# Kernel tuning notes

Measured on AMD Instinct MI355X. Metric: run time of the kernel, lower is better.

## Reference

```python
import jax, jax.numpy as jnp
import numpy as np

N = 50000   # nodes
E = 800000  # edges (avg degree 16)
D = 128     # in_dim = out_dim
H = 8       # heads
O = D // H  # per-head dim = 16
FF = 512    # ffn inner hidden
LN_EPS = 1e-6
LRELU_SLOPE = 0.01  # torch F.leaky_relu default


def setup_inputs() -> dict:
    key = jax.random.key(0)
    ks = jax.random.split(key, 9)
    x = jax.random.normal(ks[0], (N, D), jnp.float32)
    src = jax.random.randint(ks[1], (E,), 0, N)
    dst = jax.random.randint(ks[2], (E,), 0, N)
    fc_w = jax.random.normal(ks[3], (H, D, O), jnp.float32) * 0.05
    a_l = jax.random.normal(ks[4], (H, O), jnp.float32) * 0.05
    a_r = jax.random.normal(ks[5], (H, O), jnp.float32) * 0.05
    w1 = jax.random.normal(ks[6], (D, FF), jnp.float32) * 0.05
    b1 = jnp.zeros((FF,), jnp.float32)
    w2 = jax.random.normal(ks[7], (FF, D), jnp.float32) * 0.05
    b2 = jnp.zeros((D,), jnp.float32)
    ln_g = jnp.ones((D,), jnp.float32)
    ln_b = jnp.zeros((D,), jnp.float32)
    return dict(x=x, fc_w=fc_w, a_l=a_l, a_r=a_r, ln_g=ln_g, ln_b=ln_b,
                w1=w1, b1=b1, w2=w2, b2=b2, src=src, dst=dst)


def _gat_s2s(x, fc_w, a_l, a_r, src, dst):
    # per-head projection: [N,H,O]
    z = jnp.einsum('nd,hdo->nho', x, fc_w)
    # attn_fc([z_src||z_dst]) == a_l . z_src + a_r . z_dst  (decomposed, same math)
    el = jnp.einsum('nho,ho->nh', z, a_l)  # [N,H]
    er = jnp.einsum('nho,ho->nh', z, a_r)  # [N,H]
    e = jax.nn.leaky_relu(el[src] + er[dst], LRELU_SLOPE)  # [E,H]
    # edge softmax over incoming edges of each dst node (numerically stable)
    m = jax.ops.segment_max(e, dst, num_segments=N)  # [N,H]
    m = jnp.where(jnp.isfinite(m), m, 0.0)
    ex = jnp.exp(e - m[dst])  # [E,H]
    denom = jax.ops.segment_sum(ex, dst, num_segments=N)  # [N,H]
    alpha = ex / denom[dst]  # [E,H]
    # weighted aggregation of source features: [N,H,O]
    agg = jax.ops.segment_sum(alpha[:, :, None] * z[src], dst, num_segments=N)
    return agg.reshape(N, H * O)  # head concat -> [N,D]


def _ffn(h, ln_g, ln_b, w1, b1, w2, b2):
    # pre-LayerNorm positionwise FFN with gelu and residual (dropout off / eval)
    mu = jnp.mean(h, axis=-1, keepdims=True)
    var = jnp.mean((h - mu) ** 2, axis=-1, keepdims=True)
    ln = (h - mu) * jax.lax.rsqrt(var + LN_EPS) * ln_g + ln_b
    inter = jax.nn.gelu(ln @ w1 + b1, approximate=False)
    return inter @ w2 + b2 + h


def reference(x, fc_w, a_l, a_r, ln_g, ln_b, w1, b1, w2, b2, src, dst):
    h = jax.nn.elu(_gat_s2s(x, fc_w, a_l, a_r, src, dst))
    h = h + x  # residual with origin (S2S: origin == neighbor == x)
    return _ffn(h, ln_g, ln_b, w1, b1, w2, b2)
```

## Files before the change

### kernel.cpp

```cpp
#include <hip/hip_runtime.h>

#define NN 50000
#define EE 800000
#define LDK 136
#define SLOTS 64
#define FEPT 8
#define NFB 391

#define C_ZW   0
#define C_AL   16384
#define C_AR   16512
#define C_LNG  16640
#define C_LNB  16768
#define C_W1T  16896
#define C_B1   82432
#define C_W2T  82944
#define C_B2   148480
#define C_WAT  148608
#define C_TOT  150656

typedef __attribute__((ext_vector_type(8))) short bf16x8;
typedef __attribute__((ext_vector_type(4))) float f32x4;

__device__ __forceinline__ float bf2f(unsigned short u) {
  union { unsigned int i; float f; } v; v.i = ((unsigned int)u) << 16; return v.f;
}
__device__ __forceinline__ unsigned short f2bf(float f) {
  union { float f; unsigned int i; } v; v.f = f;
  unsigned int r = v.i + 0x7fffu + ((v.i >> 16) & 1u);
  return (unsigned short)(r >> 16);
}
__device__ __forceinline__ int ld_idx(const void* p, int i, int is64) {
  return is64 ? (int)((const long long*)p)[i] : ((const int*)p)[i];
}

__device__ __forceinline__ float fast_gelu(float u) {
  float ax = fabsf(u) * 0.70710678118654752f;
  float d  = fmaf(0.3275911f, ax, 1.f);
  float r  = __builtin_amdgcn_rcpf(d);
  r = r * fmaf(-d, r, 2.f);
  float p = fmaf(1.061405429f, r, -1.453152027f);
  p = fmaf(p, r, 1.421413741f);
  p = fmaf(p, r, -0.284496736f);
  p = fmaf(p, r, 0.254829592f);
  p = p * r;
  float e = __expf(-ax * ax);
  float erfv = fmaf(-p, e, 1.f);
  union { float f; unsigned int i; } su, se;
  su.f = u; se.f = erfv;
  se.i = se.i | (su.i & 0x80000000u);
  return 0.5f * u * (1.f + se.f);
}

__global__ void k_probe(const unsigned short* __restrict__ xr,
                        const int* __restrict__ s, const int* __restrict__ d,
                        int* __restrict__ flags) {
  int i = blockIdx.x * 256 + threadIdx.x;
  int bad = 0, zc = 0, zs = 0, zd = 0;
  for (int j = i; j < 65536; j += 32 * 256) {
    unsigned short u = xr[j];
    if ((u & 0x7F80u) == 0x7F80u) bad = 1;
    if (((j & 1) == 0) && u == 0) zc++;
  }
  for (int j = i; j < 131072; j += 32 * 256) {
    if (j & 1) {
      if (s[j] == 0) zs++;
      if (d[j] == 0) zd++;
    }
  }
  if (bad) atomicOr(&flags[0], 1);
  if (zc) atomicAdd(&flags[1], zc);
  if (zs) atomicAdd(&flags[2], zs);
  if (zd) atomicAdd(&flags[3], zd);
}

__global__ __launch_bounds__(256) void k_convert(
    const void* __restrict__ fcw,
    const void* __restrict__ a_l, const void* __restrict__ a_r,
    const void* __restrict__ lng, const void* __restrict__ lnb,
    const void* __restrict__ w1, const void* __restrict__ b1,
    const void* __restrict__ w2, const void* __restrict__ b2,
    const int* __restrict__ flag, unsigned short* __restrict__ canon) {
  const int isf32 = (flag[0] != 0) || (flag[1] > 8192);
  for (int i = blockIdx.x * 256 + threadIdx.x; i < C_TOT; i += gridDim.x * 256) {
    unsigned short v;
    if (i >= C_WAT) {
      int j = i - C_WAT; int c = j >> 7, dd = j & 127; int h = c & 7;
      const void* fa = (c < 8) ? a_l : a_r;
      float s = 0.f;
      if (isf32) {
        const float* fw = (const float*)fcw + h * 2048 + dd * 16;
        const float* fv = (const float*)fa + h * 16;
#pragma unroll
        for (int o = 0; o < 16; o++) s += fw[o] * fv[o];
      } else {
        const unsigned short* fw = (const unsigned short*)fcw + h * 2048 + dd * 16;
        const unsigned short* fv = (const unsigned short*)fa + h * 16;
#pragma unroll
        for (int o = 0; o < 16; o++) s += bf2f(fw[o]) * bf2f(fv[o]);
      }
      v = f2bf(s);
    } else {
      const void* src; int idx;
      if (i < C_AL)       { int c = i >> 7, d = i & 127; src = fcw; idx = (c >> 4) * 2048 + d * 16 + (c & 15); }
      else if (i < C_AR)  { src = a_l; idx = i - C_AL; }
      else if (i < C_LNG) { src = a_r; idx = i - C_AR; }
      else if (i < C_LNB) { src = lng; idx = i - C_LNG; }
      else if (i < C_W1T) { src = lnb; idx = i - C_LNB; }
      else if (i < C_B1)  { int j = i - C_W1T; int n = j >> 7, k = j & 127; src = w1; idx = k * 512 + n; }
      else if (i < C_W2T) { src = b1;  idx = i - C_B1; }
      else if (i < C_B2)  { int j = i - C_W2T; int n = j >> 9, k = j & 511; src = w2; idx = k * 128 + n; }
      else                { src = b2;  idx = i - C_B2; }
      if (isf32) v = f2bf(((const float*)src)[idx]);
      else       v = ((const unsigned short*)src)[idx];
    }
    canon[i] = v;
  }
}

__device__ __forceinline__ void do_fill(const void* __restrict__ src,
                                        const void* __restrict__ dst,
                                        const int* __restrict__ iflags,
                                        int* __restrict__ cnt,
                                        unsigned short* __restrict__ esrc,
                                        int base) {
  if (base >= EE) return;
  const int s64 = iflags[0] > 1000, d64 = iflags[1] > 1000;
  int dv[FEPT], sv[FEPT];
  if (!d64 && base + FEPT <= EE) {
    const int4* p = (const int4*)((const int*)dst + base);
    int4 a = p[0], b = p[1];
    dv[0]=a.x; dv[1]=a.y; dv[2]=a.z; dv[3]=a.w; dv[4]=b.x; dv[5]=b.y; dv[6]=b.z; dv[7]=b.w;
  } else {
#pragma unroll
    for (int j = 0; j < FEPT; j++) dv[j] = (base + j < EE) ? ld_idx(dst, base + j, d64) : 0;
  }
  if (!s64 && base + FEPT <= EE) {
    const int4* p = (const int4*)((const int*)src + base);
    int4 a = p[0], b = p[1];
    sv[0]=a.x; sv[1]=a.y; sv[2]=a.z; sv[3]=a.w; sv[4]=b.x; sv[5]=b.y; sv[6]=b.z; sv[7]=b.w;
  } else {
#pragma unroll
    for (int j = 0; j < FEPT; j++) sv[j] = (base + j < EE) ? ld_idx(src, base + j, s64) : 0;
  }
#pragma unroll
  for (int j = 0; j < FEPT; j++) {
    if (base + j < EE) {
      unsigned d = (unsigned)dv[j]; if (d >= NN) d = 0;
      unsigned s = (unsigned)sv[j]; if (s >= NN) s = 0;
      int p = atomicAdd(&cnt[d], 1);
      if (p < SLOTS) esrc[d * SLOTS + p] = (unsigned short)s;
    }
  }
}

__global__ __launch_bounds__(256) void k_projfill(
    const unsigned short* __restrict__ canon, const void* __restrict__ xraw,
    unsigned short* __restrict__ z, float* __restrict__ el, float* __restrict__ er,
    const void* __restrict__ srcp, const void* __restrict__ dstp,
    const int* __restrict__ flags,
    int* __restrict__ cnt, unsigned short* __restrict__ esrc) {
  __shared__ unsigned short sA[128 * LDK];
  __shared__ unsigned short sB[64 * LDK];
  if (blockIdx.x < NFB) {
    do_fill(srcp, dstp, flags + 2, cnt, esrc, (blockIdx.x * 256 + threadIdx.x) * FEPT);
    return;
  }
  const int pid = blockIdx.x - NFB;
  const unsigned short* zwt = canon + C_ZW;
  const unsigned short* wat = canon + C_WAT;
  const int isf32 = (flags[0] != 0) || (flags[1] > 8192);
  const int tid = threadIdx.x;
  const int row0 = (pid >> 1) * 128;
  const int n0 = (pid & 1) * 64;
  for (int v = tid; v < 2048; v += 256) {
    int r = v >> 4, k8 = (v & 15) << 3;
    int gr = row0 + r; if (gr >= NN) gr = NN - 1;
    if (isf32) {
      const float* xf = (const float*)xraw + gr * 128 + k8;
      float4 a = *(const float4*)xf;
      float4 b = *(const float4*)(xf + 4);
      union { unsigned short u[8]; uint4 q; } pk;
      pk.u[0] = f2bf(a.x); pk.u[1] = f2bf(a.y); pk.u[2] = f2bf(a.z); pk.u[3] = f2bf(a.w);
      pk.u[4] = f2bf(b.x); pk.u[5] = f2bf(b.y); pk.u[6] = f2bf(b.z); pk.u[7] = f2bf(b.w);
      *(uint4*)(&sA[r * LDK + k8]) = pk.q;
    } else {
      *(uint4*)(&sA[r * LDK + k8]) = *(const uint4*)((const unsigned short*)xraw + gr * 128 + k8);
    }
  }
  for (int v = tid; v < 1024; v += 256) {
    int n = v >> 4, k8 = (v & 15) << 3;
    *(uint4*)(&sB[n * LDK + k8]) = *(const uint4*)(zwt + (n0 + n) * 128 + k8);
  }
  __syncthreads();
  const int lane = tid & 63, w = tid >> 6;
  const int mr = lane & 15, q = lane >> 4;
  const f32x4 zero = {0.f, 0.f, 0.f, 0.f};
  f32x4 acc[8];
#pragma unroll
  for (int i = 0; i < 8; i++) acc[i] = zero;
#pragma unroll
  for (int kc = 0; kc < 4; kc++) {
    bf16x8 b = *(const bf16x8*)(&sB[(w * 16 + mr) * LDK + kc * 32 + q * 8]);
#pragma unroll
    for (int mt = 0; mt < 8; mt++) {
      bf16x8 a = *(const bf16x8*)(&sA[(mt * 16 + mr) * LDK + kc * 32 + q * 8]);
      acc[mt] = __builtin_amdgcn_mfma_f32_16x16x32_bf16(a, b, acc[mt], 0, 0, 0);
    }
  }
  const int col = n0 + w * 16 + mr;
#pragma unroll
  for (int mt = 0; mt < 8; mt++) {
#pragma unroll
    for (int r = 0; r < 4; r++) {
      int grow = row0 + mt * 16 + q * 4 + r;
      if (grow < NN) z[grow * 128 + col] = f2bf(acc[mt][r]);
    }
  }
  if (n0 == 0) {
    f32x4 e0 = zero, e1 = zero;
#pragma unroll
    for (int kc = 0; kc < 4; kc++) {
      bf16x8 b = *(const bf16x8*)(wat + mr * 128 + kc * 32 + q * 8);
      bf16x8 a0 = *(const bf16x8*)(&sA[(w * 16 + mr) * LDK + kc * 32 + q * 8]);
      bf16x8 a1 = *(const bf16x8*)(&sA[((w + 4) * 16 + mr) * LDK + kc * 32 + q * 8]);
      e0 = __builtin_amdgcn_mfma_f32_16x16x32_bf16(a0, b, e0, 0, 0, 0);
      e1 = __builtin_amdgcn_mfma_f32_16x16x32_bf16(a1, b, e1, 0, 0, 0);
    }
    float* eo = (mr < 8) ? el : er;
    const int hh = mr & 7;
#pragma unroll
    for (int r = 0; r < 4; r++) {
      int g0 = row0 + w * 16 + q * 4 + r;
      int g1 = row0 + (w + 4) * 16 + q * 4 + r;
      if (g0 < NN) eo[g0 * 8 + hh] = e0[r];
      if (g1 < NN) eo[g1 * 8 + hh] = e1[r];
    }
  }
}

__global__ __launch_bounds__(256) void k_agg(
    const void* __restrict__ xraw, const unsigned short* __restrict__ z,
    const float* __restrict__ el, const float* __restrict__ er,
    const int* __restrict__ cnt, const unsigned short* __restrict__ esrc,
    const void* __restrict__ srcp, const void* __restrict__ dstp,
    const int* __restrict__ flags,
    float* __restrict__ h1out, float2* __restrict__ mars) {
  const int lane = threadIdx.x & 63;
  const int node = blockIdx.x * 4 + (threadIdx.x >> 6);
  if (node >= NN) return;
  const int degr = cnt[node];
  const int hl = lane & 7;
  const int g  = lane >> 3;
  const float ern = er[node * 8 + hl];

  float m = -3.0e38f;
  float acc[16];
#pragma unroll
  for (int j = 0; j < 16; j++) acc[j] = 0.f;
  float denom = 0.f;

  if (degr <= SLOTS) {
    const int deg = degr;
    const unsigned short* eptr = esrc + node * SLOTS;
    for (int b = 0; b < deg; b += 16) {
      int e0 = b + g, e1 = b + g + 8;
      int c0 = (e0 < deg) ? e0 : deg - 1;
      int c1 = (e1 < deg) ? e1 : deg - 1;
      unsigned s0 = eptr[c0]; if (s0 >= NN) s0 = 0;
      unsigned s1 = eptr[c1]; if (s1 >= NN) s1 = 0;
      float t0 = el[s0 * 8 + hl] + ern;
      float t1 = el[s1 * 8 + hl] + ern;
      t0 = (t0 > 0.f) ? t0 : 0.01f * t0;
      t1 = (t1 > 0.f) ? t1 : 0.01f * t1;
      if (e0 < deg) m = fmaxf(m, t0);
      if (e1 < deg) m = fmaxf(m, t1);
    }
    m = fmaxf(m, __shfl_xor(m, 8));
    m = fmaxf(m, __shfl_xor(m, 16));
    m = fmaxf(m, __shfl_xor(m, 32));
    for (int b = 0; b < deg; b += 16) {
      int e0 = b + g, e1 = b + g + 8;
      int c0 = (e0 < deg) ? e0 : deg - 1;
      int c1 = (e1 < deg) ? e1 : deg - 1;
      unsigned s0 = eptr[c0]; if (s0 >= NN) s0 = 0;
      unsigned s1 = eptr[c1]; if (s1 >= NN) s1 = 0;
      float t0 = el[s0 * 8 + hl] + ern;
      float t1 = el[s1 * 8 + hl] + ern;
      bf16x8 za0 = *(const bf16x8*)(z + s0 * 128 + hl * 16);
      bf16x8 za1 = *(const bf16x8*)(z + s0 * 128 + hl * 16 + 8);
      bf16x8 zb0 = *(const bf16x8*)(z + s1 * 128 + hl * 16);
      bf16x8 zb1 = *(const bf16x8*)(z + s1 * 128 + hl * 16 + 8);
      t0 = (t0 > 0.f) ? t0 : 0.01f * t0;
      t1 = (t1 > 0.f) ? t1 : 0.01f * t1;
      float ex0 = (e0 < deg) ? __expf(fminf(t0 - m, 0.f)) : 0.f;
      float ex1 = (e1 < deg) ? __expf(fminf(t1 - m, 0.f)) : 0.f;
      denom += ex0 + ex1;
#pragma unroll
      for (int j = 0; j < 8; j++) {
        acc[j]     += ex0 * bf2f((unsigned short)za0[j]) + ex1 * bf2f((unsigned short)zb0[j]);
        acc[j + 8] += ex0 * bf2f((unsigned short)za1[j]) + ex1 * bf2f((unsigned short)zb1[j]);
      }
    }
  } else {
    const int s64 = flags[2] > 1000, d64 = flags[3] > 1000;
    for (int b = 0; b < EE; b += 8) {
      int e = b + g;
      unsigned dd = (unsigned)ld_idx(dstp, e, d64); if (dd >= NN) dd = 0;
      bool ok = (dd == (unsigned)node);
      unsigned s0 = (unsigned)ld_idx(srcp, e, s64); if (s0 >= NN) s0 = 0;
      float t0 = el[s0 * 8 + hl] + ern;
      t0 = (t0 > 0.f) ? t0 : 0.01f * t0;
      if (ok) m = fmaxf(m, t0);
    }
    m = fmaxf(m, __shfl_xor(m, 8));
    m = fmaxf(m, __shfl_xor(m, 16));
    m = fmaxf(m, __shfl_xor(m, 32));
    for (int b = 0; b < EE; b += 8) {
      int e = b + g;
      unsigned dd = (unsigned)ld_idx(dstp, e, d64); if (dd >= NN) dd = 0;
      bool ok = (dd == (unsigned)node);
      unsigned s0 = (unsigned)ld_idx(srcp, e, s64); if (s0 >= NN) s0 = 0;
      float t0 = el[s0 * 8 + hl] + ern;
      t0 = (t0 > 0.f) ? t0 : 0.01f * t0;
      float ex0 = ok ? __expf(fminf(t0 - m, 0.f)) : 0.f;
      denom += ex0;
      bf16x8 za0 = *(const bf16x8*)(z + s0 * 128 + hl * 16);
      bf16x8 za1 = *(const bf16x8*)(z + s0 * 128 + hl * 16 + 8);
#pragma unroll
      for (int j = 0; j < 8; j++) {
        acc[j]     += ex0 * bf2f((unsigned short)za0[j]);
        acc[j + 8] += ex0 * bf2f((unsigned short)za1[j]);
      }
    }
  }

  denom += __shfl_xor(denom, 8);
  denom += __shfl_xor(denom, 16);
  denom += __shfl_xor(denom, 32);
  {
    const bool hi1 = (lane & 32) != 0;
#pragma unroll
    for (int j = 0; j < 8; j++) {
      float send = hi1 ? acc[j] : acc[j + 8];
      float recv = __shfl_xor(send, 32);
      float keep = hi1 ? acc[j + 8] : acc[j];
      acc[j] = keep + recv;
    }
    const bool hi2 = (lane & 16) != 0;
#pragma unroll
    for (int j = 0; j < 4; j++) {
      float send = hi2 ? acc[j] : acc[j + 4];
      float recv = __shfl_xor(send, 16);
      float keep = hi2 ? acc[j + 4] : acc[j];
      acc[j] = keep + recv;
    }
    const bool hi3 = (lane & 8) != 0;
#pragma unroll
    for (int j = 0; j < 2; j++) {
      float send = hi3 ? acc[j] : acc[j + 2];
      float recv = __shfl_xor(send, 8);
      float keep = hi3 ? acc[j + 2] : acc[j];
      acc[j] = keep + recv;
    }
  }
  const float inv = (denom > 0.f) ? 1.f / denom : 0.f;
  const int c = hl * 16 + g * 2;
  float r0 = acc[0] * inv;
  float r1 = acc[1] * inv;
  float xv0, xv1;
  if ((flags[0] != 0) || (flags[1] > 8192)) {
    float2 t = *(const float2*)((const float*)xraw + (size_t)node * 128 + c);
    xv0 = t.x; xv1 = t.y;
  } else {
    unsigned int xx = *(const unsigned int*)((const unsigned short*)xraw + (size_t)node * 128 + c);
    xv0 = bf2f((unsigned short)(xx & 0xffffu));
    xv1 = bf2f((unsigned short)(xx >> 16));
  }
  float hv0 = ((r0 > 0.f) ? r0 : (__expf(fminf(r0, 0.f)) - 1.f)) + xv0;
  float hv1 = ((r1 > 0.f) ? r1 : (__expf(fminf(r1, 0.f)) - 1.f)) + xv1;
  float s1 = hv0 + hv1;
  float s2 = hv0 * hv0 + hv1 * hv1;
#pragma unroll
  for (int off = 1; off < 64; off <<= 1) {
    s1 += __shfl_xor(s1, off);
    s2 += __shfl_xor(s2, off);
  }
  if (lane == 0) {
    float mu = s1 * (1.f / 128.f);
    float var = s2 * (1.f / 128.f) - mu * mu;
    mars[node] = make_float2(mu, rsqrtf(fmaxf(var, 0.f) + 1e-6f));
  }
  *(float2*)(h1out + node * 128 + c) = make_float2(hv0, hv1);
}

__global__ __launch_bounds__(512) void k_ffn(
    const unsigned short* __restrict__ canon, const float2* __restrict__ mars,
    float* __restrict__ out) {
  const unsigned short* lngc = canon + C_LNG;
  const unsigned short* lnbc = canon + C_LNB;
  const unsigned short* w1t  = canon + C_W1T;
  const unsigned short* b1c  = canon + C_B1;
  const unsigned short* w2t  = canon + C_W2T;
  const unsigned short* b2c  = canon + C_B2;
  __shared__ unsigned short sLn[32 * LDK];
  __shared__ unsigned short sInt[32 * LDK];
  const int tid = threadIdx.x;
  const int row0 = blockIdx.x * 32;
  {
    const int r = tid >> 4, t16 = tid & 15;
    const int grow = row0 + r;
    const int gr = (grow < NN) ? grow : NN - 1;
    const float2 ms = mars[gr];
    const float* hrow = out + (size_t)gr * 128 + t16 * 8;
    float4 a = *(const float4*)(hrow);
    float4 b = *(const float4*)(hrow + 4);
    union { unsigned short u[8]; uint4 q; } gv, bv, pk;
    gv.q = *(const uint4*)(lngc + t16 * 8);
    bv.q = *(const uint4*)(lnbc + t16 * 8);
    float vv[8] = {a.x, a.y, a.z, a.w, b.x, b.y, b.z, b.w};
#pragma unroll
    for (int j = 0; j < 8; j++)
      pk.u[j] = f2bf((vv[j] - ms.x) * ms.y * bf2f(gv.u[j]) + bf2f(bv.u[j]));
    *(uint4*)(&sLn[r * LDK + t16 * 8]) = pk.q;
  }
  __syncthreads();
  const int lane = tid & 63, w = tid >> 6;
  const int mr = lane & 15, q = lane >> 4;
  const f32x4 zero = {0.f, 0.f, 0.f, 0.f};
  f32x4 acc2[2];
  acc2[0] = zero; acc2[1] = zero;
#pragma unroll
  for (int qr = 0; qr < 4; qr++) {
    if (qr) __syncthreads();
    const int colg = qr * 128 + w * 16;
    f32x4 a1[2];
    a1[0] = zero; a1[1] = zero;
#pragma unroll
    for (int kc = 0; kc < 4; kc++) {
      bf16x8 wf = *(const bf16x8*)(w1t + (colg + mr) * 128 + kc * 32 + q * 8);
#pragma unroll
      for (int rt = 0; rt < 2; rt++) {
        bf16x8 lf = *(const bf16x8*)(&sLn[(rt * 16 + mr) * LDK + kc * 32 + q * 8]);
        a1[rt] = __builtin_amdgcn_mfma_f32_16x16x32_bf16(wf, lf, a1[rt], 0, 0, 0);
      }
    }
    union { unsigned short u[4]; uint2 v; } b1v;
    b1v.v = *(const uint2*)(b1c + colg + q * 4);
#pragma unroll
    for (int rt = 0; rt < 2; rt++) {
      union { unsigned short u[4]; uint2 v; } pk;
#pragma unroll
      for (int r = 0; r < 4; r++)
        pk.u[r] = f2bf(fast_gelu(a1[rt][r] + bf2f(b1v.u[r])));
      *(uint2*)(&sInt[(rt * 16 + mr) * LDK + w * 16 + q * 4]) = pk.v;
    }
    __syncthreads();
#pragma unroll
    for (int ks = 0; ks < 4; ks++) {
      bf16x8 bw = *(const bf16x8*)(w2t + (w * 16 + mr) * 512 + qr * 128 + ks * 32 + q * 8);
#pragma unroll
      for (int mt = 0; mt < 2; mt++) {
        bf16x8 af = *(const bf16x8*)(&sInt[(mt * 16 + mr) * LDK + ks * 32 + q * 8]);
        acc2[mt] = __builtin_amdgcn_mfma_f32_16x16x32_bf16(af, bw, acc2[mt], 0, 0, 0);
      }
    }
  }
  {
    const int col = w * 16 + mr;
    const float bias = bf2f(b2c[col]);
#pragma unroll
    for (int mt = 0; mt < 2; mt++)
#pragma unroll
      for (int r = 0; r < 4; r++) {
        int grow = row0 + mt * 16 + q * 4 + r;
        if (grow < NN) {
          size_t o = (size_t)grow * 128 + col;
          out[o] = acc2[mt][r] + bias + out[o];
        }
      }
  }
}

extern "C" void kernel_launch(void* const* d_in, const int* in_sizes, int n_in,
                              void* d_out, int out_size, void* d_ws, size_t ws_size,
                              hipStream_t stream) {
  const void* x   = d_in[0];
  const void* fcw = d_in[1];
  const void* a_l = d_in[2];
  const void* a_r = d_in[3];
  const void* lng = d_in[4];
  const void* lnb = d_in[5];
  const void* w1  = d_in[6];
  const void* b1  = d_in[7];
  const void* w2  = d_in[8];
  const void* b2  = d_in[9];
  const void* src = d_in[10];
  const void* dst = d_in[11];
  float* out = (float*)d_out;

  char* ws = (char*)d_ws;
  size_t off = 0;
  auto alloc = [&](size_t bytes) -> char* {
    char* p = ws + off; off += (bytes + 255) & ~(size_t)255; return p;
  };
  int* flags            = (int*)alloc(64);
  int* cnt              = (int*)alloc((size_t)NN * 4);
  unsigned short* esrc  = (unsigned short*)alloc((size_t)NN * SLOTS * 2);
  unsigned short* canon = (unsigned short*)alloc((size_t)C_TOT * 2);
  unsigned short* z     = (unsigned short*)alloc((size_t)NN * 128 * 2);
  float* el             = (float*)alloc((size_t)NN * 8 * 4);
  float* er             = (float*)alloc((size_t)NN * 8 * 4);
  float2* mars          = (float2*)alloc((size_t)NN * 8);

  hipMemsetAsync(ws, 0, 256 + (size_t)NN * 4, stream);
  k_probe<<<32, 256, 0, stream>>>((const unsigned short*)x, (const int*)src, (const int*)dst, flags);
  k_convert<<<256, 256, 0, stream>>>(fcw, a_l, a_r, lng, lnb, w1, b1, w2, b2, flags, canon);
  k_projfill<<<NFB + 391 * 2, 256, 0, stream>>>(canon, x, z, el, er, src, dst, flags, cnt, esrc);
  k_agg<<<(NN + 3) / 4, 256, 0, stream>>>(x, z, el, er, cnt, esrc, src, dst, flags, out, mars);
  k_ffn<<<(NN + 31) / 32, 512, 0, stream>>>(canon, mars, out);
}
```

Measured before the change: 261.1 us.

## Fuse GAT aggregation with LayerNorm and FFN in one 64-row kernel

Merges the aggregation and FFN kernels. Each 512-thread block first aggregates 64 nodes (8 per wave, looping serially), applying ELU, the residual and LayerNorm, and writes the normalized rows straight to shared memory as bf16. It then runs the two MFMA GEMMs on a 64-row tile instead of 32. This removes the mars buffer, one kernel launch, and the re-read of h from global memory. In exchange, each wave now handles nodes one after another, which lowers parallelism and latency hiding in the gather-heavy phase, and the launch has far fewer blocks (782).

```diff
diff --git a/kernel.cpp b/kernel.cpp
--- a/kernel.cpp
+++ b/kernel.cpp
@@ -239,208 +239,192 @@
   }
 }
 
-__global__ __launch_bounds__(256) void k_agg(
-    const void* __restrict__ xraw, const unsigned short* __restrict__ z,
+__global__ __launch_bounds__(512) void k_aggffn(
+    const unsigned short* __restrict__ canon, const void* __restrict__ xraw,
+    const unsigned short* __restrict__ z,
     const float* __restrict__ el, const float* __restrict__ er,
     const int* __restrict__ cnt, const unsigned short* __restrict__ esrc,
     const void* __restrict__ srcp, const void* __restrict__ dstp,
-    const int* __restrict__ flags,
-    float* __restrict__ h1out, float2* __restrict__ mars) {
-  const int lane = threadIdx.x & 63;
-  const int node = blockIdx.x * 4 + (threadIdx.x >> 6);
-  if (node >= NN) return;
-  const int degr = cnt[node];
+    const int* __restrict__ flags, float* __restrict__ out) {
+  __shared__ unsigned short sLn[64 * LDK];
+  __shared__ unsigned short sInt[64 * LDK];
+  const int tid = threadIdx.x;
+  const int lane = tid & 63, w = tid >> 6;
+  const int row0 = blockIdx.x * 64;
   const int hl = lane & 7;
   const int g  = lane >> 3;
-  const float ern = er[node * 8 + hl];
-
-  float m = -3.0e38f;
-  float acc[16];
-#pragma unroll
-  for (int j = 0; j < 16; j++) acc[j] = 0.f;
-  float denom = 0.f;
-
-  if (degr <= SLOTS) {
-    const int deg = degr;
-    const unsigned short* eptr = esrc + node * SLOTS;
-    for (int b = 0; b < deg; b += 16) {
-      int e0 = b + g, e1 = b + g + 8;
-      int c0 = (e0 < deg) ? e0 : deg - 1;
-      int c1 = (e1 < deg) ? e1 : deg - 1;
-      unsigned s0 = eptr[c0]; if (s0 >= NN) s0 = 0;
-      unsigned s1 = eptr[c1]; if (s1 >= NN) s1 = 0;
-      float t0 = el[s0 * 8 + hl] + ern;
-      float t1 = el[s1 * 8 + hl] + ern;
-      t0 = (t0 > 0.f) ? t0 : 0.01f * t0;
-      t1 = (t1 > 0.f) ? t1 : 0.01f * t1;
-      if (e0 < deg) m = fmaxf(m, t0);
-      if (e1 < deg) m = fmaxf(m, t1);
-    }
-    m = fmaxf(m, __shfl_xor(m, 8));
-    m = fmaxf(m, __shfl_xor(m, 16));
-    m = fmaxf(m, __shfl_xor(m, 32));
-    for (int b = 0; b < deg; b += 16) {
-      int e0 = b + g, e1 = b + g + 8;
-      int c0 = (e0 < deg) ? e0 : deg - 1;
-      int c1 = (e1 < deg) ? e1 : deg - 1;
-      unsigned s0 = eptr[c0]; if (s0 >= NN) s0 = 0;
-      unsigned s1 = eptr[c1]; if (s1 >= NN) s1 = 0;
-      float t0 = el[s0 * 8 + hl] + ern;
-      float t1 = el[s1 * 8 + hl] + ern;
-      bf16x8 za0 = *(const bf16x8*)(z + s0 * 128 + hl * 16);
-      bf16x8 za1 = *(const bf16x8*)(z + s0 * 128 + hl * 16 + 8);
-      bf16x8 zb0 = *(const bf16x8*)(z + s1 * 128 + hl * 16);
-      bf16x8 zb1 = *(const bf16x8*)(z + s1 * 128 + hl * 16 + 8);
-      t0 = (t0 > 0.f) ? t0 : 0.01f * t0;
-      t1 = (t1 > 0.f) ? t1 : 0.01f * t1;
-      float ex0 = (e0 < deg) ? __expf(fminf(t0 - m, 0.f)) : 0.f;
-      float ex1 = (e1 < deg) ? __expf(fminf(t1 - m, 0.f)) : 0.f;
-      denom += ex0 + ex1;
+  const int c  = hl * 16 + g * 2;
+  const int isf32x = (flags[0] != 0) || (flags[1] > 8192);
+  unsigned int gq = *(const unsigned int*)(canon + C_LNG + c);
+  unsigned int bq = *(const unsigned int*)(canon + C_LNB + c);
+  const float g0 = bf2f((unsigned short)(gq & 0xffffu)), g1 = bf2f((unsigned short)(gq >> 16));
+  const float b0 = bf2f((unsigned short)(bq & 0xffffu)), b1 = bf2f((unsigned short)(bq >> 16));
+  for (int nn = 0; nn < 8; nn++) {
+    const int node0 = row0 + w * 8 + nn;
+    const int node = (node0 < NN) ? node0 : NN - 1;
+    const int degr = cnt[node];
+    const float ern = er[node * 8 + hl];
+    float m = -3.0e38f;
+    float acc[16];
+#pragma unroll
+    for (int j = 0; j < 16; j++) acc[j] = 0.f;
+    float denom = 0.f;
+    if (degr <= SLOTS) {
+      const int deg = degr;
+      const unsigned short* eptr = esrc + node * SLOTS;
+      for (int b = 0; b < deg; b += 16) {
+        int e0 = b + g, e1 = b + g + 8;
+        int c0 = (e0 < deg) ? e0 : deg - 1;
+        int c1 = (e1 < deg) ? e1 : deg - 1;
+        unsigned s0 = eptr[c0]; if (s0 >= NN) s0 = 0;
+        unsigned s1 = eptr[c1]; if (s1 >= NN) s1 = 0;
+        float t0 = el[s0 * 8 + hl] + ern;
+        float t1 = el[s1 * 8 + hl] + ern;
+        t0 = (t0 > 0.f) ? t0 : 0.01f * t0;
+        t1 = (t1 > 0.f) ? t1 : 0.01f * t1;
+        if (e0 < deg) m = fmaxf(m, t0);
+        if (e1 < deg) m = fmaxf(m, t1);
+      }
+      m = fmaxf(m, __shfl_xor(m, 8));
+      m = fmaxf(m, __shfl_xor(m, 16));
+      m = fmaxf(m, __shfl_xor(m, 32));
+      for (int b = 0; b < deg; b += 16) {
+        int e0 = b + g, e1 = b + g + 8;
+        int c0 = (e0 < deg) ? e0 : deg - 1;
+        int c1 = (e1 < deg) ? e1 : deg - 1;
+        unsigned s0 = eptr[c0]; if (s0 >= NN) s0 = 0;
+        unsigned s1 = eptr[c1]; if (s1 >= NN) s1 = 0;
+        float t0 = el[s0 * 8 + hl] + ern;
+        float t1 = el[s1 * 8 + hl] + ern;
+        bf16x8 za0 = *(const bf16x8*)(z + s0 * 128 + hl * 16);
+        bf16x8 za1 = *(const bf16x8*)(z + s0 * 128 + hl * 16 + 8);
+        bf16x8 zb0 = *(const bf16x8*)(z + s1 * 128 + hl * 16);
+        bf16x8 zb1 = *(const bf16x8*)(z + s1 * 128 + hl * 16 + 8);
+        t0 = (t0 > 0.f) ? t0 : 0.01f * t0;
+        t1 = (t1 > 0.f) ? t1 : 0.01f * t1;
+        float ex0 = (e0 < deg) ? __expf(fminf(t0 - m, 0.f)) : 0.f;
+        float ex1 = (e1 < deg) ? __expf(fminf(t1 - m, 0.f)) : 0.f;
+        denom += ex0 + ex1;
+#pragma unroll
+        for (int j = 0; j < 8; j++) {
+          acc[j]     += ex0 * bf2f((unsigned short)za0[j]) + ex1 * bf2f((unsigned short)zb0[j]);
+          acc[j + 8] += ex0 * bf2f((unsigned short)za1[j]) + ex1 * bf2f((unsigned short)zb1[j]);
+        }
+      }
+    } else {
+      const int s64 = flags[2] > 1000, d64 = flags[3] > 1000;
+      for (int b = 0; b < EE; b += 8) {
+        int e = b + g;
+        unsigned dd = (unsigned)ld_idx(dstp, e, d64); if (dd >= NN) dd = 0;
+        bool ok = (dd == (unsigned)node);
+        unsigned s0 = (unsigned)ld_idx(srcp, e, s64); if (s0 >= NN) s0 = 0;
+        float t0 = el[s0 * 8 + hl] + ern;
+        t0 = (t0 > 0.f) ? t0 : 0.01f * t0;
+        if (ok) m = fmaxf(m, t0);
+      }
+      m = fmaxf(m, __shfl_xor(m, 8));
+      m = fmaxf(m, __shfl_xor(m, 16));
+      m = fmaxf(m, __shfl_xor(m, 32));
+      for (int b = 0; b < EE; b += 8) {
+        int e = b + g;
+        unsigned dd = (unsigned)ld_idx(dstp, e, d64); if (dd >= NN) dd = 0;
+        bool ok = (dd == (unsigned)node);
+        unsigned s0 = (unsigned)ld_idx(srcp, e, s64); if (s0 >= NN) s0 = 0;
+        float t0 = el[s0 * 8 + hl] + ern;
+        t0 = (t0 > 0.f) ? t0 : 0.01f * t0;
+        float ex0 = ok ? __expf(fminf(t0 - m, 0.f)) : 0.f;
+        denom += ex0;
+        bf16x8 za0 = *(const bf16x8*)(z + s0 * 128 + hl * 16);
+        bf16x8 za1 = *(const bf16x8*)(z + s0 * 128 + hl * 16 + 8);
+#pragma unroll
+        for (int j = 0; j < 8; j++) {
+          acc[j]     += ex0 * bf2f((unsigned short)za0[j]);
+          acc[j + 8] += ex0 * bf2f((unsigned short)za1[j]);
+        }
+      }
+    }
+    denom += __shfl_xor(denom, 8);
+    denom += __shfl_xor(denom, 16);
+    denom += __shfl_xor(denom, 32);
+    {
+      const bool hi1 = (lane & 32) != 0;
 #pragma unroll
       for (int j = 0; j < 8; j++) {
-        acc[j]     += ex0 * bf2f((unsigned short)za0[j]) + ex1 * bf2f((unsigned short)zb0[j]);
-        acc[j + 8] += ex0 * bf2f((unsigned short)za1[j]) + ex1 * bf2f((unsigned short)zb1[j]);
-      }
-    }
-  } else {
-    const int s64 = flags[2] > 1000, d64 = flags[3] > 1000;
-    for (int b = 0; b < EE; b += 8) {
-      int e = b + g;
-      unsigned dd = (unsigned)ld_idx(dstp, e, d64); if (dd >= NN) dd = 0;
-      bool ok = (dd == (unsigned)node);
-      unsigned s0 = (unsigned)ld_idx(srcp, e, s64); if (s0 >= NN) s0 = 0;
-      float t0 = el[s0 * 8 + hl] + ern;
-      t0 = (t0 > 0.f) ? t0 : 0.01f * t0;
-      if (ok) m = fmaxf(m, t0);
-    }
-    m = fmaxf(m, __shfl_xor(m, 8));
-    m = fmaxf(m, __shfl_xor(m, 16));
-    m = fmaxf(m, __shfl_xor(m, 32));
-    for (int b = 0; b < EE; b += 8) {
-      int e = b + g;
-      unsigned dd = (unsigned)ld_idx(dstp, e, d64); if (dd >= NN) dd = 0;
-      bool ok = (dd == (unsigned)node);
-      unsigned s0 = (unsigned)ld_idx(srcp, e, s64); if (s0 >= NN) s0 = 0;
-      float t0 = el[s0 * 8 + hl] + ern;
-      t0 = (t0 > 0.f) ? t0 : 0.01f * t0;
-      float ex0 = ok ? __expf(fminf(t0 - m, 0.f)) : 0.f;
-      denom += ex0;
-      bf16x8 za0 = *(const bf16x8*)(z + s0 * 128 + hl * 16);
-      bf16x8 za1 = *(const bf16x8*)(z + s0 * 128 + hl * 16 + 8);
-#pragma unroll
-      for (int j = 0; j < 8; j++) {
-        acc[j]     += ex0 * bf2f((unsigned short)za0[j]);
-        acc[j + 8] += ex0 * bf2f((unsigned short)za1[j]);
-      }
-    }
-  }
-
-  denom += __shfl_xor(denom, 8);
-  denom += __shfl_xor(denom, 16);
-  denom += __shfl_xor(denom, 32);
-  {
-    const bool hi1 = (lane & 32) != 0;
-#pragma unroll
-    for (int j = 0; j < 8; j++) {
-      float send = hi1 ? acc[j] : acc[j + 8];
-      float recv = __shfl_xor(send, 32);
-      float keep = hi1 ? acc[j + 8] : acc[j];
-      acc[j] = keep + recv;
-    }
-    const bool hi2 = (lane & 16) != 0;
-#pragma unroll
-    for (int j = 0; j < 4; j++) {
-      float send = hi2 ? acc[j] : acc[j + 4];
-      float recv = __shfl_xor(send, 16);
-      float keep = hi2 ? acc[j + 4] : acc[j];
-      acc[j] = keep + recv;
-    }
-    const bool hi3 = (lane & 8) != 0;
-#pragma unroll
-    for (int j = 0; j < 2; j++) {
-      float send = hi3 ? acc[j] : acc[j + 2];
-      float recv = __shfl_xor(send, 8);
-      float keep = hi3 ? acc[j + 2] : acc[j];
-      acc[j] = keep + recv;
-    }
-  }
-  const float inv = (denom > 0.f) ? 1.f / denom : 0.f;
-  const int c = hl * 16 + g * 2;
-  float r0 = acc[0] * inv;
-  float r1 = acc[1] * inv;
-  float xv0, xv1;
-  if ((flags[0] != 0) || (flags[1] > 8192)) {
-    float2 t = *(const float2*)((const float*)xraw + (size_t)node * 128 + c);
-    xv0 = t.x; xv1 = t.y;
-  } else {
-    unsigned int xx = *(const unsigned int*)((const unsigned short*)xraw + (size_t)node * 128 + c);
-    xv0 = bf2f((unsigned short)(xx & 0xffffu));
-    xv1 = bf2f((unsigned short)(xx >> 16));
-  }
-  float hv0 = ((r0 > 0.f) ? r0 : (__expf(fminf(r0, 0.f)) - 1.f)) + xv0;
-  float hv1 = ((r1 > 0.f) ? r1 : (__expf(fminf(r1, 0.f)) - 1.f)) + xv1;
-  float s1 = hv0 + hv1;
-  float s2 = hv0 * hv0 + hv1 * hv1;
-#pragma unroll
-  for (int off = 1; off < 64; off <<= 1) {
-    s1 += __shfl_xor(s1, off);
-    s2 += __shfl_xor(s2, off);
-  }
-  if (lane == 0) {
-    float mu = s1 * (1.f / 128.f);
-    float var = s2 * (1.f / 128.f) - mu * mu;
-    mars[node] = make_float2(mu, rsqrtf(fmaxf(var, 0.f) + 1e-6f));
-  }
-  *(float2*)(h1out + node * 128 + c) = make_float2(hv0, hv1);
-}
-
-__global__ __launch_bounds__(512) void k_ffn(
-    const unsigned short* __restrict__ canon, const float2* __restrict__ mars,
-    float* __restrict__ out) {
-  const unsigned short* lngc = canon + C_LNG;
-  const unsigned short* lnbc = canon + C_LNB;
-  const unsigned short* w1t  = canon + C_W1T;
-  const unsigned short* b1c  = canon + C_B1;
-  const unsigned short* w2t  = canon + C_W2T;
-  const unsigned short* b2c  = canon + C_B2;
-  __shared__ unsigned short sLn[32 * LDK];
-  __shared__ unsigned short sInt[32 * LDK];
-  const int tid = threadIdx.x;
-  const int row0 = blockIdx.x * 32;
-  {
-    const int r = tid >> 4, t16 = tid & 15;
-    const int grow = row0 + r;
-    const int gr = (grow < NN) ? grow : NN - 1;
-    const float2 ms = mars[gr];
-    const float* hrow = out + (size_t)gr * 128 + t16 * 8;
-    float4 a = *(const float4*)(hrow);
-    float4 b = *(const float4*)(hrow + 4);
-    union { unsigned short u[8]; uint4 q; } gv, bv, pk;
-    gv.q = *(const uint4*)(lngc + t16 * 8);
-    bv.q = *(const uint4*)(lnbc + t16 * 8);
-    float vv[8] = {a.x, a.y, a.z, a.w, b.x, b.y, b.z, b.w};
-#pragma unroll
-    for (int j = 0; j < 8; j++)
-      pk.u[j] = f2bf((vv[j] - ms.x) * ms.y * bf2f(gv.u[j]) + bf2f(bv.u[j]));
-    *(uint4*)(&sLn[r * LDK + t16 * 8]) = pk.q;
+        float send = hi1 ? acc[j] : acc[j + 8];
+        float recv = __shfl_xor(send, 32);
+        float keep = hi1 ? acc[j + 8] : acc[j];
+        acc[j] = keep + recv;
+      }
+      const bool hi2 = (lane & 16) != 0;
+#pragma unroll
+      for (int j = 0; j < 4; j++) {
+        float send = hi2 ? acc[j] : acc[j + 4];
+        float recv = __shfl_xor(send, 16);
+        float keep = hi2 ? acc[j + 4] : acc[j];
+        acc[j] = keep + recv;
+      }
+      const bool hi3 = (lane & 8) != 0;
+#pragma unroll
+      for (int j = 0; j < 2; j++) {
+        float send = hi3 ? acc[j] : acc[j + 2];
+        float recv = __shfl_xor(send, 8);
+        float keep = hi3 ? acc[j + 2] : acc[j];
+        acc[j] = keep + recv;
+      }
+    }
+    const float inv = (denom > 0.f) ? 1.f / denom : 0.f;
+    float r0 = acc[0] * inv;
+    float r1 = acc[1] * inv;
+    float xv0, xv1;
+    if (isf32x) {
+      float2 t = *(const float2*)((const float*)xraw + (size_t)node * 128 + c);
+      xv0 = t.x; xv1 = t.y;
+    } else {
+      unsigned int xx = *(const unsigned int*)((const unsigned short*)xraw + (size_t)node * 128 + c);
+      xv0 = bf2f((unsigned short)(xx & 0xffffu));
+      xv1 = bf2f((unsigned short)(xx >> 16));
+    }
+    float hv0 = ((r0 > 0.f) ? r0 : (__expf(fminf(r0, 0.f)) - 1.f)) + xv0;
+    float hv1 = ((r1 > 0.f) ? r1 : (__expf(fminf(r1, 0.f)) - 1.f)) + xv1;
+    float s1 = hv0 + hv1;
+    float s2 = hv0 * hv0 + hv1 * hv1;
+#pragma unroll
+    for (int off = 1; off < 64; off <<= 1) {
+      s1 += __shfl_xor(s1, off);
+      s2 += __shfl_xor(s2, off);
+    }
+    const float mu = s1 * (1.f / 128.f);
+    const float var = s2 * (1.f / 128.f) - mu * mu;
+    const float rs = rsqrtf(fmaxf(var, 0.f) + 1e-6f);
+    if (node0 < NN)
+      *(float2*)(out + (size_t)node0 * 128 + c) = make_float2(hv0, hv1);
+    union { unsigned short u[2]; unsigned int q; } pk;
+    pk.u[0] = f2bf((hv0 - mu) * rs * g0 + b0);
+    pk.u[1] = f2bf((hv1 - mu) * rs * g1 + b1);
+    *(unsigned int*)(&sLn[(w * 8 + nn) * LDK + c]) = pk.q;
   }
   __syncthreads();
-  const int lane = tid & 63, w = tid >> 6;
+  const unsigned short* w1t = canon + C_W1T;
+  const unsigned short* b1c = canon + C_B1;
+  const unsigned short* w2t = canon + C_W2T;
+  const unsigned short* b2c = canon + C_B2;
   const int mr = lane & 15, q = lane >> 4;
   const f32x4 zero = {0.f, 0.f, 0.f, 0.f};
-  f32x4 acc2[2];
-  acc2[0] = zero; acc2[1] = zero;
+  f32x4 acc2[4];
+#pragma unroll
+  for (int a = 0; a < 4; a++) acc2[a] = zero;
 #pragma unroll
   for (int qr = 0; qr < 4; qr++) {
     if (qr) __syncthreads();
     const int colg = qr * 128 + w * 16;
-    f32x4 a1[2];
-    a1[0] = zero; a1[1] = zero;
+    f32x4 a1[4];
+#pragma unroll
+    for (int a = 0; a < 4; a++) a1[a] = zero;
 #pragma unroll
     for (int kc = 0; kc < 4; kc++) {
       bf16x8 wf = *(const bf16x8*)(w1t + (colg + mr) * 128 + kc * 32 + q * 8);
 #pragma unroll
-      for (int rt = 0; rt < 2; rt++) {
+      for (int rt = 0; rt < 4; rt++) {
         bf16x8 lf = *(const bf16x8*)(&sLn[(rt * 16 + mr) * LDK + kc * 32 + q * 8]);
         a1[rt] = __builtin_amdgcn_mfma_f32_16x16x32_bf16(wf, lf, a1[rt], 0, 0, 0);
       }
@@ -448,7 +432,7 @@
     union { unsigned short u[4]; uint2 v; } b1v;
     b1v.v = *(const uint2*)(b1c + colg + q * 4);
 #pragma unroll
-    for (int rt = 0; rt < 2; rt++) {
+    for (int rt = 0; rt < 4; rt++) {
       union { unsigned short u[4]; uint2 v; } pk;
 #pragma unroll
       for (int r = 0; r < 4; r++)
@@ -460,7 +444,7 @@
     for (int ks = 0; ks < 4; ks++) {
       bf16x8 bw = *(const bf16x8*)(w2t + (w * 16 + mr) * 512 + qr * 128 + ks * 32 + q * 8);
 #pragma unroll
-      for (int mt = 0; mt < 2; mt++) {
+      for (int mt = 0; mt < 4; mt++) {
         bf16x8 af = *(const bf16x8*)(&sInt[(mt * 16 + mr) * LDK + ks * 32 + q * 8]);
         acc2[mt] = __builtin_amdgcn_mfma_f32_16x16x32_bf16(af, bw, acc2[mt], 0, 0, 0);
       }
@@ -470,7 +454,7 @@
     const int col = w * 16 + mr;
     const float bias = bf2f(b2c[col]);
 #pragma unroll
-    for (int mt = 0; mt < 2; mt++)
+    for (int mt = 0; mt < 4; mt++)
 #pragma unroll
       for (int r = 0; r < 4; r++) {
         int grow = row0 + mt * 16 + q * 4 + r;
@@ -511,12 +495,10 @@
   unsigned short* z     = (unsigned short*)alloc((size_t)NN * 128 * 2);
   float* el             = (float*)alloc((size_t)NN * 8 * 4);
   float* er             = (float*)alloc((size_t)NN * 8 * 4);
-  float2* mars          = (float2*)alloc((size_t)NN * 8);
 
   hipMemsetAsync(ws, 0, 256 + (size_t)NN * 4, stream);
   k_probe<<<32, 256, 0, stream>>>((const unsigned short*)x, (const int*)src, (const int*)dst, flags);
   k_convert<<<256, 256, 0, stream>>>(fcw, a_l, a_r, lng, lnb, w1, b1, w2, b2, flags, canon);
   k_projfill<<<NFB + 391 * 2, 256, 0, stream>>>(canon, x, z, el, er, src, dst, flags, cnt, esrc);
-  k_agg<<<(NN + 3) / 4, 256, 0, stream>>>(x, z, el, er, cnt, esrc, src, dst, flags, out, mars);
-  k_ffn<<<(NN + 31) / 32, 512, 0, stream>>>(canon, mars, out);
-}
+  k_aggffn<<<(NN + 63) / 64, 512, 0, stream>>>(canon, x, z, el, er, cnt, esrc, src, dst, flags, out);
+}
```

New measurement: 282.1 us. 1.08x slower.

## Overlap FFN of first node half with aggregation of second half

Applied to the files above, without the earlier changes.

Splits aggregation into two halves and launches a mixed kernel where some blocks run the FFN on the first half of nodes while the other blocks aggregate the second half; a final kernel runs the FFN on the second half. The FFN tile grows from 32 to 64 rows per block, doubling reuse of each loaded weight fragment. Aggregation blocks now hold 8 waves. The goal is to overlap MFMA-heavy FFN work with memory-bound gather work, at the cost of an extra launch and large LDS allocation in the mixed kernel that can limit occupancy of its aggregation blocks.

```diff
diff --git a/kernel.cpp b/kernel.cpp
--- a/kernel.cpp
+++ b/kernel.cpp
@@ -6,6 +6,11 @@
 #define SLOTS 64
 #define FEPT 8
 #define NFB 391
+#define M1 25024
+#define A1B 3128
+#define A2B 3122
+#define F1B 391
+#define F2B 391
 
 #define C_ZW   0
 #define C_AL   16384
@@ -239,16 +244,15 @@
   }
 }
 
-__global__ __launch_bounds__(256) void k_agg(
+__device__ __forceinline__ void agg_wave(
     const void* __restrict__ xraw, const unsigned short* __restrict__ z,
     const float* __restrict__ el, const float* __restrict__ er,
     const int* __restrict__ cnt, const unsigned short* __restrict__ esrc,
     const void* __restrict__ srcp, const void* __restrict__ dstp,
     const int* __restrict__ flags,
-    float* __restrict__ h1out, float2* __restrict__ mars) {
+    float* __restrict__ h1out, float2* __restrict__ mars, int node) {
+  if (node < 0 || node >= NN) return;
   const int lane = threadIdx.x & 63;
-  const int node = blockIdx.x * 4 + (threadIdx.x >> 6);
-  if (node >= NN) return;
   const int degr = cnt[node];
   const int hl = lane & 7;
   const int g  = lane >> 3;
@@ -394,53 +398,55 @@
   *(float2*)(h1out + node * 128 + c) = make_float2(hv0, hv1);
 }
 
-__global__ __launch_bounds__(512) void k_ffn(
+__device__ __forceinline__ void ffn_rows(
     const unsigned short* __restrict__ canon, const float2* __restrict__ mars,
-    float* __restrict__ out) {
+    float* __restrict__ out, int row0, unsigned short* sLn, unsigned short* sInt) {
   const unsigned short* lngc = canon + C_LNG;
   const unsigned short* lnbc = canon + C_LNB;
   const unsigned short* w1t  = canon + C_W1T;
   const unsigned short* b1c  = canon + C_B1;
   const unsigned short* w2t  = canon + C_W2T;
   const unsigned short* b2c  = canon + C_B2;
-  __shared__ unsigned short sLn[32 * LDK];
-  __shared__ unsigned short sInt[32 * LDK];
   const int tid = threadIdx.x;
-  const int row0 = blockIdx.x * 32;
   {
-    const int r = tid >> 4, t16 = tid & 15;
+    const int r = tid >> 3, t8 = tid & 7;
     const int grow = row0 + r;
     const int gr = (grow < NN) ? grow : NN - 1;
     const float2 ms = mars[gr];
-    const float* hrow = out + (size_t)gr * 128 + t16 * 8;
-    float4 a = *(const float4*)(hrow);
-    float4 b = *(const float4*)(hrow + 4);
-    union { unsigned short u[8]; uint4 q; } gv, bv, pk;
-    gv.q = *(const uint4*)(lngc + t16 * 8);
-    bv.q = *(const uint4*)(lnbc + t16 * 8);
-    float vv[8] = {a.x, a.y, a.z, a.w, b.x, b.y, b.z, b.w};
-#pragma unroll
-    for (int j = 0; j < 8; j++)
-      pk.u[j] = f2bf((vv[j] - ms.x) * ms.y * bf2f(gv.u[j]) + bf2f(bv.u[j]));
-    *(uint4*)(&sLn[r * LDK + t16 * 8]) = pk.q;
+    const float* hrow = out + (size_t)gr * 128 + t8 * 16;
+#pragma unroll
+    for (int h8 = 0; h8 < 2; h8++) {
+      float4 a = *(const float4*)(hrow + h8 * 8);
+      float4 b = *(const float4*)(hrow + h8 * 8 + 4);
+      union { unsigned short u[8]; uint4 q; } gv, bv, pk;
+      gv.q = *(const uint4*)(lngc + t8 * 16 + h8 * 8);
+      bv.q = *(const uint4*)(lnbc + t8 * 16 + h8 * 8);
+      float vv[8] = {a.x, a.y, a.z, a.w, b.x, b.y, b.z, b.w};
+#pragma unroll
+      for (int j = 0; j < 8; j++)
+        pk.u[j] = f2bf((vv[j] - ms.x) * ms.y * bf2f(gv.u[j]) + bf2f(bv.u[j]));
+      *(uint4*)(&sLn[r * LDK + t8 * 16 + h8 * 8]) = pk.q;
+    }
   }
   __syncthreads();
   const int lane = tid & 63, w = tid >> 6;
   const int mr = lane & 15, q = lane >> 4;
   const f32x4 zero = {0.f, 0.f, 0.f, 0.f};
-  f32x4 acc2[2];
-  acc2[0] = zero; acc2[1] = zero;
+  f32x4 acc2[4];
+#pragma unroll
+  for (int a = 0; a < 4; a++) acc2[a] = zero;
 #pragma unroll
   for (int qr = 0; qr < 4; qr++) {
     if (qr) __syncthreads();
     const int colg = qr * 128 + w * 16;
-    f32x4 a1[2];
-    a1[0] = zero; a1[1] = zero;
+    f32x4 a1[4];
+#pragma unroll
+    for (int a = 0; a < 4; a++) a1[a] = zero;
 #pragma unroll
     for (int kc = 0; kc < 4; kc++) {
       bf16x8 wf = *(const bf16x8*)(w1t + (colg + mr) * 128 + kc * 32 + q * 8);
 #pragma unroll
-      for (int rt = 0; rt < 2; rt++) {
+      for (int rt = 0; rt < 4; rt++) {
         bf16x8 lf = *(const bf16x8*)(&sLn[(rt * 16 + mr) * LDK + kc * 32 + q * 8]);
         a1[rt] = __builtin_amdgcn_mfma_f32_16x16x32_bf16(wf, lf, a1[rt], 0, 0, 0);
       }
@@ -448,7 +454,7 @@
     union { unsigned short u[4]; uint2 v; } b1v;
     b1v.v = *(const uint2*)(b1c + colg + q * 4);
 #pragma unroll
-    for (int rt = 0; rt < 2; rt++) {
+    for (int rt = 0; rt < 4; rt++) {
       union { unsigned short u[4]; uint2 v; } pk;
 #pragma unroll
       for (int r = 0; r < 4; r++)
@@ -460,7 +466,7 @@
     for (int ks = 0; ks < 4; ks++) {
       bf16x8 bw = *(const bf16x8*)(w2t + (w * 16 + mr) * 512 + qr * 128 + ks * 32 + q * 8);
 #pragma unroll
-      for (int mt = 0; mt < 2; mt++) {
+      for (int mt = 0; mt < 4; mt++) {
         bf16x8 af = *(const bf16x8*)(&sInt[(mt * 16 + mr) * LDK + ks * 32 + q * 8]);
         acc2[mt] = __builtin_amdgcn_mfma_f32_16x16x32_bf16(af, bw, acc2[mt], 0, 0, 0);
       }
@@ -470,7 +476,7 @@
     const int col = w * 16 + mr;
     const float bias = bf2f(b2c[col]);
 #pragma unroll
-    for (int mt = 0; mt < 2; mt++)
+    for (int mt = 0; mt < 4; mt++)
 #pragma unroll
       for (int r = 0; r < 4; r++) {
         int grow = row0 + mt * 16 + q * 4 + r;
@@ -480,6 +486,44 @@
         }
       }
   }
+}
+
+__global__ __launch_bounds__(512) void k_agg8(
+    const void* __restrict__ xraw, const unsigned short* __restrict__ z,
+    const float* __restrict__ el, const float* __restrict__ er,
+    const int* __restrict__ cnt, const unsigned short* __restrict__ esrc,
+    const void* __restrict__ srcp, const void* __restrict__ dstp,
+    const int* __restrict__ flags,
+    float* __restrict__ out, float2* __restrict__ mars) {
+  const int node = blockIdx.x * 8 + (threadIdx.x >> 6);
+  agg_wave(xraw, z, el, er, cnt, esrc, srcp, dstp, flags, out, mars,
+           (node < M1) ? node : -1);
+}
+
+__global__ __launch_bounds__(512) void k_mix(
+    const unsigned short* __restrict__ canon, const void* __restrict__ xraw,
+    const unsigned short* __restrict__ z,
+    const float* __restrict__ el, const float* __restrict__ er,
+    const int* __restrict__ cnt, const unsigned short* __restrict__ esrc,
+    const void* __restrict__ srcp, const void* __restrict__ dstp,
+    const int* __restrict__ flags,
+    float* __restrict__ out, float2* __restrict__ mars) {
+  __shared__ unsigned short sLn[64 * LDK];
+  __shared__ unsigned short sInt[64 * LDK];
+  if (blockIdx.x < F1B) {
+    ffn_rows(canon, mars, out, blockIdx.x * 64, sLn, sInt);
+    return;
+  }
+  const int node = M1 + (blockIdx.x - F1B) * 8 + (threadIdx.x >> 6);
+  agg_wave(xraw, z, el, er, cnt, esrc, srcp, dstp, flags, out, mars, node);
+}
+
+__global__ __launch_bounds__(512) void k_ffn64(
+    const unsigned short* __restrict__ canon, const float2* __restrict__ mars,
+    float* __restrict__ out) {
+  __shared__ unsigned short sLn[64 * LDK];
+  __shared__ unsigned short sInt[64 * LDK];
+  ffn_rows(canon, mars, out, M1 + blockIdx.x * 64, sLn, sInt);
 }
 
 extern "C" void kernel_launch(void* const* d_in, const int* in_sizes, int n_in,
@@ -517,6 +561,7 @@
   k_probe<<<32, 256, 0, stream>>>((const unsigned short*)x, (const int*)src, (const int*)dst, flags);
   k_convert<<<256, 256, 0, stream>>>(fcw, a_l, a_r, lng, lnb, w1, b1, w2, b2, flags, canon);
   k_projfill<<<NFB + 391 * 2, 256, 0, stream>>>(canon, x, z, el, er, src, dst, flags, cnt, esrc);
-  k_agg<<<(NN + 3) / 4, 256, 0, stream>>>(x, z, el, er, cnt, esrc, src, dst, flags, out, mars);
-  k_ffn<<<(NN + 31) / 32, 512, 0, stream>>>(canon, mars, out);
-}
+  k_agg8<<<A1B, 512, 0, stream>>>(x, z, el, er, cnt, esrc, src, dst, flags, out, mars);
+  k_mix<<<F1B + A2B, 512, 0, stream>>>(canon, x, z, el, er, cnt, esrc, src, dst, flags, out, mars);
+  k_ffn64<<<F2B, 512, 0, stream>>>(canon, mars, out);
+}
```

Result: slower. 266.6 us (+2.1%).
